# Performance work log

Measured on AMD Instinct MI355X. Metric: run time of the kernel, lower is better.

Reference implementation:

```python
import jax, jax.numpy as jnp
import numpy as np

N, T, D, H = 256, 512, 256, 256


def setup_inputs() -> dict:
    key = jax.random.key(0)
    ks = jax.random.split(key, 9)
    scale_x = float(np.sqrt(6.0 / (D + H)))  # xavier_uniform range approx
    scale_h = float(np.sqrt(6.0 / (H + H)))
    def wx(k):
        return jax.random.uniform(k, (D, H), jnp.float32, -scale_x, scale_x)
    def wh(k):
        return jax.random.uniform(k, (H, H), jnp.float32, -scale_h, scale_h)
    inp = {
        'x': jax.random.normal(ks[0], (N, T, D), jnp.float32),
        'w_ii': wx(ks[1]), 'w_hi': wh(ks[2]),
        'w_if': wx(ks[3]), 'w_hf': wh(ks[4]),
        'w_ig': wx(ks[5]), 'w_hg': wh(ks[6]),
        'w_io': wx(ks[7]), 'w_ho': wh(ks[8]),
        # init_hidden() zeros all 1-D params
        'b_ii': jnp.zeros((H,), jnp.float32), 'b_hi': jnp.zeros((H,), jnp.float32),
        'b_if': jnp.zeros((H,), jnp.float32), 'b_hf': jnp.zeros((H,), jnp.float32),
        'b_ig': jnp.zeros((H,), jnp.float32), 'b_hg': jnp.zeros((H,), jnp.float32),
        'b_io': jnp.zeros((H,), jnp.float32), 'b_ho': jnp.zeros((H,), jnp.float32),
    }
    return inp


def reference(x, w_ii, w_hi, w_if, w_hf, w_ig, w_hg, w_io, w_ho,
              b_ii, b_hi, b_if, b_hf, b_ig, b_hg, b_io, b_ho):
    # Fuse the 4 input projections and 4 hidden projections into 2 GEMMs
    # (mathematically identical to the 8 separate matmuls).
    Wx = jnp.concatenate([w_ii, w_if, w_ig, w_io], axis=1)  # (D, 4H)
    Wh = jnp.concatenate([w_hi, w_hf, w_hg, w_ho], axis=1)  # (H, 4H)
    b = jnp.concatenate([b_ii + b_hi, b_if + b_hf, b_ig + b_hg, b_io + b_ho])  # (4H,)
    n, t, _ = x.shape
    h = x.shape[2]  # noqa (not used)
    # Precompute input projections for all timesteps: (T, N, 4H)
    xW = jnp.einsum('ntd,dg->tng', x, Wx)
    h0 = jnp.zeros((n, w_hi.shape[0]), x.dtype)
    c0 = jnp.zeros_like(h0)

    def step(carry, xw_t):
        h_t, c_t = carry
        gates = xw_t + h_t @ Wh + b  # (N, 4H)
        i_t, f_t, g_t, o_t = jnp.split(gates, 4, axis=1)
        i_t = jax.nn.sigmoid(i_t)
        f_t = jax.nn.sigmoid(f_t)
        g_t = jnp.tanh(g_t)
        o_t = jax.nn.sigmoid(o_t)
        c_t = f_t * c_t + i_t * g_t
        h_t = o_t * jnp.tanh(c_t)
        return (h_t, c_t), None

    (h_T, c_T), _ = jax.lax.scan(step, (h0, c0), xW)
    return (h_T, c_T)
```

## Files before the change

### kernel.cpp

```cpp
#include <hip/hip_runtime.h>
#include <cstdint>

typedef float  f32x4  __attribute__((ext_vector_type(4)));
typedef __bf16 bf16x8 __attribute__((ext_vector_type(8)));
typedef int    i32x4  __attribute__((ext_vector_type(4)));
typedef unsigned short u16;
typedef u16 u16x4 __attribute__((ext_vector_type(4)));

#define TT 512

__device__ __forceinline__ u16 f2bf(float f) {
  unsigned u = __builtin_bit_cast(unsigned, f);
  unsigned r = u + 0x7fffu + ((u >> 16) & 1u);
  return (u16)(r >> 16);
}
__device__ __forceinline__ float bflo(unsigned d) { return __builtin_bit_cast(float, d << 16); }
__device__ __forceinline__ float bfhi(unsigned d) { return __builtin_bit_cast(float, d & 0xffff0000u); }
__device__ __forceinline__ float rcpf(float x) { return __builtin_amdgcn_rcpf(x); }
__device__ __forceinline__ float fsig(float x) { return rcpf(1.f + __expf(-x)); }
__device__ __forceinline__ float ftanh(float x) { return 1.f - 2.f * rcpf(1.f + __expf(2.f * x)); }
__device__ __forceinline__ void gload_lds16(const u16* g, u16* l) {
  __builtin_amdgcn_global_load_lds((const __attribute__((address_space(1))) void*)(g),
                                   (__attribute__((address_space(3))) void*)(l), 16, 0, 0);
}

__global__ __launch_bounds__(256) void prep_x(const float* __restrict__ x, u16* __restrict__ xb) {
  long o = ((long)blockIdx.x * 256 + threadIdx.x) * 4;
  int d = (int)(o & 255);
  int n = (int)((o >> 8) & 255);
  int t = (int)(o >> 16);
  const float4 v = *(const float4*)(x + ((long)n << 17) + ((long)t << 8) + d);
  u16x4 p;
  p[0] = f2bf(v.x); p[1] = f2bf(v.y); p[2] = f2bf(v.z); p[3] = f2bf(v.w);
  *(u16x4*)(xb + o) = p;
}

__global__ __launch_bounds__(256) void prep_w(
    const float* __restrict__ wii, const float* __restrict__ whi,
    const float* __restrict__ wif, const float* __restrict__ whf,
    const float* __restrict__ wig, const float* __restrict__ whg,
    const float* __restrict__ wio, const float* __restrict__ who,
    const float* __restrict__ bii, const float* __restrict__ bhi,
    const float* __restrict__ bif, const float* __restrict__ bhf,
    const float* __restrict__ big_, const float* __restrict__ bhg,
    const float* __restrict__ bio, const float* __restrict__ bho,
    u16* __restrict__ Wxb, signed char* __restrict__ Whq,
    float* __restrict__ wscale, float* __restrict__ bsum) {
  __shared__ float red[256];
  int b = blockIdx.x;
  int tid = threadIdx.x;
  if (b < 1024) {
    const float* wx[4] = {wii, wif, wig, wio};
    int G = b >> 8, h = b & 255;
    Wxb[b * 256 + tid] = f2bf(wx[G][tid * 256 + h]);
  } else if (b < 2048) {
    const float* wh[4] = {whi, whf, whg, who};
    int cidx = b - 1024;
    int G = cidx >> 8, h = cidx & 255;
    float w = wh[G][tid * 256 + h];
    red[tid] = fabsf(w);
    __syncthreads();
    for (int s = 128; s > 0; s >>= 1) {
      if (tid < s) red[tid] = fmaxf(red[tid], red[tid + s]);
      __syncthreads();
    }
    float mx = red[0];
    float scale = (mx > 0.f) ? mx * (1.f / 127.f) : 1.f;
    float qf = rintf(w / scale);
    qf = fminf(127.f, fmaxf(-127.f, qf));
    Whq[cidx * 256 + tid] = (signed char)(int)qf;
    if (tid == 0) wscale[cidx] = scale * (1.f / 127.f);
  } else {
    const float* bx[4] = {bii, bif, big_, bio};
    const float* bh[4] = {bhi, bhf, bhg, bho};
    for (int G = 0; G < 4; ++G) bsum[G * 256 + tid] = bx[G][tid] + bh[G][tid];
  }
}

__global__ __launch_bounds__(256) void gemm_xw(const u16* __restrict__ A, const u16* __restrict__ Bt,
                                               const float* __restrict__ bias, u16* __restrict__ xWp) {
  __shared__ u16 As[128 * 32];
  __shared__ u16 Bs[128 * 32];
  int bid = blockIdx.x;
  int bm = bid & 1023, bn = bid >> 10;
  int tid = threadIdx.x;
  int l = tid & 63, w = tid >> 6;
  int wm = w >> 1, wn = w & 1;
  f32x4 acc[4][4];
#pragma unroll
  for (int i = 0; i < 4; ++i)
#pragma unroll
    for (int j = 0; j < 4; ++j) acc[i][j] = (f32x4){0.f, 0.f, 0.f, 0.f};

  const u16* Ab = A + (size_t)bm * 128 * 256;
  const u16* Bb = Bt + (size_t)bn * 128 * 256;
  int row = tid >> 2;
  int ch = tid & 3;
  for (int ko = 0; ko < 8; ++ko) {
    __syncthreads();
    gload_lds16(Ab + (size_t)row * 256 + ko * 32 + ch * 8, As + tid * 8);
    gload_lds16(Ab + (size_t)(row + 64) * 256 + ko * 32 + ch * 8, As + 2048 + tid * 8);
    gload_lds16(Bb + (size_t)row * 256 + ko * 32 + ch * 8, Bs + tid * 8);
    gload_lds16(Bb + (size_t)(row + 64) * 256 + ko * 32 + ch * 8, Bs + 2048 + tid * 8);
    __syncthreads();
    bf16x8 af[4], bfr[4];
#pragma unroll
    for (int mt = 0; mt < 4; ++mt)
      af[mt] = *reinterpret_cast<const bf16x8*>(As + (wm * 64 + mt * 16 + (l & 15)) * 32 + (l >> 4) * 8);
#pragma unroll
    for (int nt = 0; nt < 4; ++nt)
      bfr[nt] = *reinterpret_cast<const bf16x8*>(Bs + (wn * 64 + nt * 16 + (l & 15)) * 32 + (l >> 4) * 8);
#pragma unroll
    for (int mt = 0; mt < 4; ++mt)
#pragma unroll
      for (int nt = 0; nt < 4; ++nt)
        acc[mt][nt] = __builtin_amdgcn_mfma_f32_16x16x32_bf16(af[mt], bfr[nt], acc[mt][nt], 0, 0, 0);
  }
#pragma unroll
  for (int mt = 0; mt < 4; ++mt) {
    int tm = bm * 8 + wm * 4 + mt;
#pragma unroll
    for (int nt = 0; nt < 4; ++nt) {
      int tn = bn * 8 + wn * 4 + nt;
      float bv = bias[tn * 16 + (l & 15)];
      u16x4 pk;
#pragma unroll
      for (int r = 0; r < 4; ++r) pk[r] = f2bf(acc[mt][nt][r] + bv);
      *reinterpret_cast<u16x4*>(xWp + ((size_t)(tm * 64 + tn) * 256 + l * 4)) = pk;
    }
  }
}

__global__ __launch_bounds__(512, 2) void lstm_rec(const signed char* __restrict__ Whq,
                                                   const float* __restrict__ wscale,
                                                   const u16* __restrict__ xWp,
                                                   float* __restrict__ out) {
  __shared__ __align__(16) signed char hb[2][576];
  int p = blockIdx.x;
  int xcd = p & 7, q8 = (p >> 3) & 7, tsel = p >> 6;
  int G = xcd * 2 + tsel;
  int tid = threadIdx.x;
  int wid = tid >> 6, l = tid & 63;
  int c = l & 15, q = (l >> 4) & 3;
  int tt = q >> 1, rsel = q & 1;

  for (int i = tid; i < 288; i += 512) ((int*)hb)[i] = 0;

  i32x4 bw[4][2][4];
#pragma unroll
  for (int g = 0; g < 4; ++g)
#pragma unroll
    for (int ttl = 0; ttl < 2; ++ttl) {
      int col = g * 256 + wid * 32 + ttl * 16 + c;
#pragma unroll
      for (int ks = 0; ks < 4; ++ks)
        bw[g][ttl][ks] = *reinterpret_cast<const i32x4*>(Whq + (size_t)col * 256 + ks * 64 + q * 16);
    }
  float sc8[4];
#pragma unroll
  for (int g = 0; g < 4; ++g) sc8[g] = wscale[g * 256 + wid * 32 + tt * 16 + c];

  const char* xbase = (const char*)xWp + (size_t)G * 32768;
  int xoff[4];
#pragma unroll
  for (int g = 0; g < 4; ++g) {
    int tn = g * 16 + wid * 2 + tt;
    xoff[g] = tn * 512 + (((q8 >> 1) * 16 + c) * 8) + (q8 & 1) * 4;
  }
  unsigned xw0[4], xw1[4];
#pragma unroll
  for (int g = 0; g < 4; ++g) xw0[g] = *(const unsigned*)(xbase + xoff[g]);
  xbase += 524288;

  i32x4 zacc = (i32x4){0, 0, 0, 0};
  float cs = 0.f, hh = 0.f;
  __syncthreads();

#define STEP(CUR, XW_CUR, XW_NXT)                                               \
  {                                                                             \
    _Pragma("unroll")                                                           \
    for (int g = 0; g < 4; ++g) XW_NXT[g] = *(const unsigned*)(xbase + xoff[g]);\
    const signed char* hr = hb[CUR ^ 1];                                        \
    i32x4 acc[4][2];                                                            \
    {                                                                           \
      i32x4 a0 = *(const i32x4*)(hr + (c & 1) * 288 + q * 16);                  \
      _Pragma("unroll")                                                         \
      for (int g = 0; g < 4; ++g) {                                             \
        __asm__("v_mfma_i32_16x16x64_i8 %0, %1, %2, %3"                         \
                : "=&v"(acc[g][0]) : "v"(a0), "a"(bw[g][0][0]), "v"(zacc));     \
        __asm__("v_mfma_i32_16x16x64_i8 %0, %1, %2, %3"                         \
                : "=&v"(acc[g][1]) : "v"(a0), "a"(bw[g][1][0]), "v"(zacc));     \
      }                                                                         \
    }                                                                           \
    _Pragma("unroll")                                                           \
    for (int ks = 1; ks < 4; ++ks) {                                            \
      i32x4 a = *(const i32x4*)(hr + (c & 1) * 288 + ks * 64 + q * 16);         \
      _Pragma("unroll")                                                         \
      for (int g = 0; g < 4; ++g) {                                             \
        __asm__("v_mfma_i32_16x16x64_i8 %0, %1, %2, %0"                         \
                : "+v"(acc[g][0]) : "v"(a), "a"(bw[g][0][ks]));                 \
        __asm__("v_mfma_i32_16x16x64_i8 %0, %1, %2, %0"                         \
                : "+v"(acc[g][1]) : "v"(a), "a"(bw[g][1][ks]));                 \
      }                                                                         \
    }                                                                           \
    __asm__ volatile("s_nop 7\n\ts_nop 7\n\ts_nop 7");   \
    float a4[4];                                                                \
    _Pragma("unroll")                                                           \
    for (int g = 0; g < 4; ++g) {                                               \
      int e = tt ? (rsel ? acc[g][1][1] : acc[g][1][0])                         \
                 : (rsel ? acc[g][0][1] : acc[g][0][0]);                        \
      unsigned d = XW_CUR[g];                                                   \
      float xv = rsel ? bfhi(d) : bflo(d);                                      \
      a4[g] = (float)e * sc8[g] + xv;                                           \
    }                                                                           \
    float gi = fsig(a4[0]);                                                     \
    float gf = fsig(a4[1]);                                                     \
    float gg = ftanh(a4[2]);                                                    \
    float go = fsig(a4[3]);                                                     \
    cs = gf * cs + gi * gg;                                                     \
    hh = go * ftanh(cs);                                                        \
    int hq = (int)rintf(hh * 127.f);                                            \
    hb[CUR][rsel * 288 + wid * 32 + tt * 16 + c] = (signed char)hq;             \
    xbase += 524288;                                                            \
    __builtin_amdgcn_s_waitcnt(0xC07F);   \
    __builtin_amdgcn_s_barrier();                                               \
  }

  for (int t = 0; t < TT; t += 2) {
    STEP(0, xw0, xw1)
    STEP(1, xw1, xw0)
  }
#undef STEP

  {
    int n = G * 16 + q8 * 2 + rsel;
    int hu = wid * 32 + tt * 16 + c;
    out[(size_t)n * 256 + hu] = hh;
    out[65536 + (size_t)n * 256 + hu] = cs;
  }
}

extern "C" void kernel_launch(void* const* d_in, const int* in_sizes, int n_in,
                              void* d_out, int out_size, void* d_ws, size_t ws_size,
                              hipStream_t stream) {
  const float* x   = (const float*)d_in[0];
  const float* wii = (const float*)d_in[1];
  const float* whi = (const float*)d_in[2];
  const float* wif = (const float*)d_in[3];
  const float* whf = (const float*)d_in[4];
  const float* wig = (const float*)d_in[5];
  const float* whg = (const float*)d_in[6];
  const float* wio = (const float*)d_in[7];
  const float* who = (const float*)d_in[8];
  const float* bii = (const float*)d_in[9];
  const float* bhi = (const float*)d_in[10];
  const float* bif = (const float*)d_in[11];
  const float* bhf = (const float*)d_in[12];
  const float* big_ = (const float*)d_in[13];
  const float* bhg = (const float*)d_in[14];
  const float* bio = (const float*)d_in[15];
  const float* bho = (const float*)d_in[16];

  char* ws = (char*)d_ws;
  u16*   xb     = (u16*)(ws);
  u16*   Wxb    = (u16*)(ws + 67108864);
  signed char* Whq = (signed char*)(ws + 67633152);
  float* wscale = (float*)(ws + 67895296);
  float* bsum   = (float*)(ws + 67899392);
  u16*   xWp    = (u16*)(ws + 67903488);
  float* out = (float*)d_out;

  prep_x<<<32768, 256, 0, stream>>>(x, xb);
  prep_w<<<2049, 256, 0, stream>>>(wii, whi, wif, whf, wig, whg, wio, who,
                                   bii, bhi, bif, bhf, big_, bhg, bio, bho,
                                   Wxb, Whq, wscale, bsum);
  gemm_xw<<<8192, 256, 0, stream>>>(xb, Wxb, bsum, xWp);
  lstm_rec<<<128, 512, 0, stream>>>(Whq, wscale, xWp, out);
}
```

Measured before the change: 745.1 us.

## Fuse x bf16 conversion into input-projection GEMM with resident A tile

Removes the separate prep_x kernel and its intermediate bf16 buffer: each GEMM block now reads fp32 x directly, converts to bf16, and keeps its full 128x256 A panel in swizzled LDS. The block then loops over all eight N tiles, streaming double-buffered B slices via global-to-LDS loads, so A is read from global memory once instead of eight times. This trades a 64KB+ LDS footprint and fewer, longer blocks (1024 instead of 8192) for less global traffic and one fewer launch.

```diff
diff --git a/kernel.cpp b/kernel.cpp
--- a/kernel.cpp
+++ b/kernel.cpp
@@ -22,17 +22,6 @@
 __device__ __forceinline__ void gload_lds16(const u16* g, u16* l) {
   __builtin_amdgcn_global_load_lds((const __attribute__((address_space(1))) void*)(g),
                                    (__attribute__((address_space(3))) void*)(l), 16, 0, 0);
-}
-
-__global__ __launch_bounds__(256) void prep_x(const float* __restrict__ x, u16* __restrict__ xb) {
-  long o = ((long)blockIdx.x * 256 + threadIdx.x) * 4;
-  int d = (int)(o & 255);
-  int n = (int)((o >> 8) & 255);
-  int t = (int)(o >> 16);
-  const float4 v = *(const float4*)(x + ((long)n << 17) + ((long)t << 8) + d);
-  u16x4 p;
-  p[0] = f2bf(v.x); p[1] = f2bf(v.y); p[2] = f2bf(v.z); p[3] = f2bf(v.w);
-  *(u16x4*)(xb + o) = p;
 }
 
 __global__ __launch_bounds__(256) void prep_w(
@@ -77,56 +66,90 @@
   }
 }
 
-__global__ __launch_bounds__(256) void gemm_xw(const u16* __restrict__ A, const u16* __restrict__ Bt,
-                                               const float* __restrict__ bias, u16* __restrict__ xWp) {
-  __shared__ u16 As[128 * 32];
-  __shared__ u16 Bs[128 * 32];
-  int bid = blockIdx.x;
-  int bm = bid & 1023, bn = bid >> 10;
+__global__ __launch_bounds__(256, 2) void gemm_xw(const float* __restrict__ X, const u16* __restrict__ Bt,
+                                                  const float* __restrict__ bias, u16* __restrict__ xWp) {
+  __shared__ u16 As[128 * 256];
+  __shared__ u16 Bs[2][128 * 32];
+  int bm = blockIdx.x;
   int tid = threadIdx.x;
   int l = tid & 63, w = tid >> 6;
   int wm = w >> 1, wn = w & 1;
+  int c = l & 15, q = l >> 4;
+
+  {
+    int trow = tid >> 2, ch = tid & 3;
+    gload_lds16(Bt + (size_t)trow * 256 + ch * 8, &Bs[0][0] + tid * 8);
+    gload_lds16(Bt + (size_t)(trow + 64) * 256 + ch * 8, &Bs[0][0] + 2048 + tid * 8);
+  }
+  {
+#pragma unroll 4
+    for (int j = 0; j < 32; ++j) {
+      int row_l = j * 4 + (tid >> 6);
+      int d = (tid & 63) * 4;
+      int r = bm * 128 + row_l;
+      int t = r >> 8, n = r & 255;
+      const float4 v = *(const float4*)(X + ((size_t)n * 512 + t) * 256 + d);
+      u16x4 p;
+      p[0] = f2bf(v.x); p[1] = f2bf(v.y); p[2] = f2bf(v.z); p[3] = f2bf(v.w);
+      int ba = (row_l * 512 + d * 2) ^ ((row_l & 7) << 4);
+      *(u16x4*)((char*)As + ba) = p;
+    }
+  }
+  __syncthreads();
+
   f32x4 acc[4][4];
 #pragma unroll
   for (int i = 0; i < 4; ++i)
 #pragma unroll
     for (int j = 0; j < 4; ++j) acc[i][j] = (f32x4){0.f, 0.f, 0.f, 0.f};
 
-  const u16* Ab = A + (size_t)bm * 128 * 256;
-  const u16* Bb = Bt + (size_t)bn * 128 * 256;
-  int row = tid >> 2;
-  int ch = tid & 3;
-  for (int ko = 0; ko < 8; ++ko) {
-    __syncthreads();
-    gload_lds16(Ab + (size_t)row * 256 + ko * 32 + ch * 8, As + tid * 8);
-    gload_lds16(Ab + (size_t)(row + 64) * 256 + ko * 32 + ch * 8, As + 2048 + tid * 8);
-    gload_lds16(Bb + (size_t)row * 256 + ko * 32 + ch * 8, Bs + tid * 8);
-    gload_lds16(Bb + (size_t)(row + 64) * 256 + ko * 32 + ch * 8, Bs + 2048 + tid * 8);
-    __syncthreads();
-    bf16x8 af[4], bfr[4];
-#pragma unroll
-    for (int mt = 0; mt < 4; ++mt)
-      af[mt] = *reinterpret_cast<const bf16x8*>(As + (wm * 64 + mt * 16 + (l & 15)) * 32 + (l >> 4) * 8);
-#pragma unroll
-    for (int nt = 0; nt < 4; ++nt)
-      bfr[nt] = *reinterpret_cast<const bf16x8*>(Bs + (wn * 64 + nt * 16 + (l & 15)) * 32 + (l >> 4) * 8);
-#pragma unroll
-    for (int mt = 0; mt < 4; ++mt)
+  int sw = (c & 7) << 4;
+  int rowbase[4];
+#pragma unroll
+  for (int mt = 0; mt < 4; ++mt)
+    rowbase[mt] = (wm * 64 + mt * 16 + c) * 512;
+
+  for (int bn = 0; bn < 8; ++bn) {
+#pragma unroll
+    for (int ko = 0; ko < 8; ++ko) {
+      int sn = bn * 8 + ko + 1;
+      if (sn < 64) {
+        int bnn = sn >> 3, kon = sn & 7;
+        const u16* Bb = Bt + (size_t)(bnn * 128) * 256 + kon * 32;
+        u16* dst = &Bs[(ko + 1) & 1][0];
+        int trow = tid >> 2, ch = tid & 3;
+        gload_lds16(Bb + (size_t)trow * 256 + ch * 8, dst + tid * 8);
+        gload_lds16(Bb + (size_t)(trow + 64) * 256 + ch * 8, dst + 2048 + tid * 8);
+      }
+      bf16x8 af[4], bfr[4];
+      const u16* bp = &Bs[ko & 1][0];
+      int koff = (ko * 64 + q * 16) ^ sw;
+#pragma unroll
+      for (int mt = 0; mt < 4; ++mt)
+        af[mt] = *(const bf16x8*)((const char*)As + rowbase[mt] + koff);
 #pragma unroll
       for (int nt = 0; nt < 4; ++nt)
-        acc[mt][nt] = __builtin_amdgcn_mfma_f32_16x16x32_bf16(af[mt], bfr[nt], acc[mt][nt], 0, 0, 0);
-  }
-#pragma unroll
-  for (int mt = 0; mt < 4; ++mt) {
-    int tm = bm * 8 + wm * 4 + mt;
-#pragma unroll
-    for (int nt = 0; nt < 4; ++nt) {
-      int tn = bn * 8 + wn * 4 + nt;
-      float bv = bias[tn * 16 + (l & 15)];
-      u16x4 pk;
-#pragma unroll
-      for (int r = 0; r < 4; ++r) pk[r] = f2bf(acc[mt][nt][r] + bv);
-      *reinterpret_cast<u16x4*>(xWp + ((size_t)(tm * 64 + tn) * 256 + l * 4)) = pk;
+        bfr[nt] = *(const bf16x8*)(bp + (wn * 64 + nt * 16 + c) * 32 + q * 8);
+#pragma unroll
+      for (int mt = 0; mt < 4; ++mt)
+#pragma unroll
+        for (int nt = 0; nt < 4; ++nt)
+          acc[mt][nt] = __builtin_amdgcn_mfma_f32_16x16x32_bf16(af[mt], bfr[nt], acc[mt][nt], 0, 0, 0);
+      __syncthreads();
+    }
+#pragma unroll
+    for (int mt = 0; mt < 4; ++mt) {
+      int tm = bm * 8 + wm * 4 + mt;
+#pragma unroll
+      for (int nt = 0; nt < 4; ++nt) {
+        int tn = bn * 8 + wn * 4 + nt;
+        float bv = bias[tn * 16 + c];
+        u16x4 pk;
+#pragma unroll
+        for (int r = 0; r < 4; ++r) pk[r] = f2bf(acc[mt][nt][r] + bv);
+        *reinterpret_cast<u16x4*>(xWp + ((size_t)(tm * 64 + tn) * 256 + l * 4)) = pk;
+        acc[mt][nt] = (f32x4){0.f, 0.f, 0.f, 0.f};
+      }
     }
   }
 }
@@ -262,7 +285,6 @@
   const float* bho = (const float*)d_in[16];
 
   char* ws = (char*)d_ws;
-  u16*   xb     = (u16*)(ws);
   u16*   Wxb    = (u16*)(ws + 67108864);
   signed char* Whq = (signed char*)(ws + 67633152);
   float* wscale = (float*)(ws + 67895296);
@@ -270,10 +292,9 @@
   u16*   xWp    = (u16*)(ws + 67903488);
   float* out = (float*)d_out;
 
-  prep_x<<<32768, 256, 0, stream>>>(x, xb);
   prep_w<<<2049, 256, 0, stream>>>(wii, whi, wif, whf, wig, whg, wio, who,
                                    bii, bhi, bif, bhf, big_, bhg, bio, bho,
                                    Wxb, Whq, wscale, bsum);
-  gemm_xw<<<8192, 256, 0, stream>>>(xb, Wxb, bsum, xWp);
+  gemm_xw<<<1024, 256, 0, stream>>>(x, Wxb, bsum, xWp);
   lstm_rec<<<128, 512, 0, stream>>>(Whq, wscale, xWp, out);
 }
```

Measured after the change: 692.0 us. 7.1% less time.
